# Kernel optimization log

Measured on AMD Instinct MI355X. Metric: run time of the kernel, lower is better.

The kernel has to match this reference:

```python
import jax, jax.numpy as jnp
import numpy as np

N_KW, N_RT = 100000, 20000
D, H, O = 128, 128, 128
E_A, E_B, E_C = 1600000, 1600000, 320000


def setup_inputs() -> dict:
    key = jax.random.key(0)
    ks = jax.random.split(key, 32)
    inp = {
        "x_kw": jax.random.normal(ks[0], (N_KW, D), jnp.float32),
        "x_rt": jax.random.normal(ks[1], (N_RT, D), jnp.float32),
        "src_a": jax.random.randint(ks[2], (E_A,), 0, N_RT),
        "dst_a": jax.random.randint(ks[3], (E_A,), 0, N_KW),
        "src_b": jax.random.randint(ks[4], (E_B,), 0, N_KW),
        "dst_b": jax.random.randint(ks[5], (E_B,), 0, N_KW),
        "src_c": jax.random.randint(ks[6], (E_C,), 0, N_RT),
        "dst_c": jax.random.randint(ks[7], (E_C,), 0, N_RT),
    }
    # SAGEConv params per relation per layer: W_l (neighbor), b_l, W_r (root, no bias)
    i = 8
    dims = {1: (D, H), 2: (H, O)}
    for layer in (1, 2):
        din, dout = dims[layer]
        for rel in ("a", "b", "c"):
            inp[f"Wl{layer}{rel}"] = jax.random.normal(ks[i], (din, dout), jnp.float32) * 0.05; i += 1
            inp[f"bl{layer}{rel}"] = jnp.zeros((dout,), jnp.float32)
            inp[f"Wr{layer}{rel}"] = jax.random.normal(ks[i], (din, dout), jnp.float32) * 0.05; i += 1
    return inp


def _sage(x_src, x_dst, src, dst, Wl, bl, Wr):
    # PyG SAGEConv (mean aggr): lin_l(mean_j x_src[j]) + lin_r(x_dst)
    n = x_dst.shape[0]
    s = jax.ops.segment_sum(x_src[src], dst, num_segments=n)      # [n, din]
    cnt = jax.ops.segment_sum(jnp.ones_like(dst, dtype=x_src.dtype), dst, num_segments=n)
    mean = s / jnp.maximum(cnt, 1.0)[:, None]
    return mean @ Wl + bl + x_dst @ Wr


def reference(x_kw, x_rt, src_a, dst_a, src_b, dst_b, src_c, dst_c,
              Wl1a, bl1a, Wr1a, Wl1b, bl1b, Wr1b, Wl1c, bl1c, Wr1c,
              Wl2a, bl2a, Wr2a, Wl2b, bl2b, Wr2b, Wl2c, bl2c, Wr2c):
    # layer 1 (HeteroConv aggr='sum' over relations sharing a dst type)
    kw1 = (_sage(x_rt, x_kw, src_a, dst_a, Wl1a, bl1a, Wr1a)
           + _sage(x_kw, x_kw, src_b, dst_b, Wl1b, bl1b, Wr1b))
    rt1 = _sage(x_rt, x_rt, src_c, dst_c, Wl1c, bl1c, Wr1c)
    kw1 = jax.nn.relu(kw1)
    rt1 = jax.nn.relu(rt1)
    # layer 2
    kw2 = (_sage(rt1, kw1, src_a, dst_a, Wl2a, bl2a, Wr2a)
           + _sage(kw1, kw1, src_b, dst_b, Wl2b, bl2b, Wr2b))
    rt2 = _sage(rt1, rt1, src_c, dst_c, Wl2c, bl2c, Wr2c)
    return kw2, rt2
```

## Files before the change

### kernel.cpp

```cpp
#include <hip/hip_runtime.h>

typedef __attribute__((ext_vector_type(8))) short bf16x8;
typedef __attribute__((ext_vector_type(4))) float f32x4;
typedef __attribute__((ext_vector_type(2))) float f32x2;

static __device__ __forceinline__ unsigned short f2bf(float f) {
    unsigned int u = __float_as_uint(f);
    u += 0x7fffu + ((u >> 16) & 1u);
    return (unsigned short)(u >> 16);
}
static __device__ __forceinline__ float bf2f(unsigned short h) {
    return __uint_as_float(((unsigned int)h) << 16);
}

#define BSH 6
#define BUCKET 64
#define NBMAX 1600
#define CHSH 13


struct Rel {
    const int* src; const int* dst; int E; int nb; int Ndst;
    int hblk0, hnblk;
    int sblk0, snblk;
    int oblk0;
    int shift;
    int* bcnt; int* boff; int* bcur;
    unsigned* pairs; unsigned* ssrc; int* goff; float* invd;
};
struct Rels { Rel r[3]; };

struct PrepArgs {
    const float* W[10];
    const float* Wa[10];
    const float* b1a; const float* b1b; const float* b2a; const float* b2b;
};


__global__ void prep_hist_k(PrepArgs pa, unsigned short* __restrict__ Wt,
                            float* __restrict__ bc1, float* __restrict__ bc2,
                            Rels R, int prepBlocks) {
    int bid = blockIdx.x;
    if (bid < prepBlocks) {
        if (bid < 640) {
            int slot = bid >> 6;
            int i = ((bid & 63) << 8) + threadIdx.x;
            float v = pa.W[slot][i];
            const float* w2 = pa.Wa[slot];
            if (w2) v += w2[i];
            int k = i >> 7, n = i & 127;
            Wt[slot * 16384 + n * 128 + k] = f2bf(v);
        } else {
            int t = threadIdx.x;
            if (t < 128) bc1[t] = pa.b1a[t] + pa.b1b[t];
            else bc2[t - 128] = pa.b2a[t - 128] + pa.b2b[t - 128];
        }
        return;
    }
    int hb = bid - prepBlocks;
    const Rel* r;
    if (hb < R.r[1].hblk0) r = &R.r[0];
    else if (hb < R.r[2].hblk0) r = &R.r[1];
    else r = &R.r[2];
    __shared__ int h[NBMAX];
    for (int i = threadIdx.x; i < r->nb; i += 256) h[i] = 0;
    __syncthreads();
    for (int e = (hb - r->hblk0) * 256 + threadIdx.x; e < r->E; e += r->hnblk * 256)
        atomicAdd(&h[r->dst[e] >> BSH], 1);
    __syncthreads();
    for (int i = threadIdx.x; i < r->nb; i += 256)
        if (h[i]) atomicAdd(&r->bcnt[i], h[i]);
}


__global__ void bscan3_k(Rels R) {
    const Rel* r = &R.r[blockIdx.x];
    __shared__ int s[1024];
    int t = threadIdx.x;
    int nb = r->nb;
    int e0 = 2 * t, e1 = 2 * t + 1;
    int v0 = (e0 < nb) ? r->bcnt[e0] : 0;
    int v1 = (e1 < nb) ? r->bcnt[e1] : 0;
    s[t] = v0 + v1;
    __syncthreads();
    for (int o = 1; o < 1024; o <<= 1) {
        int x = (t >= o) ? s[t - o] : 0;
        __syncthreads();
        s[t] += x;
        __syncthreads();
    }
    int P = s[t] - (v0 + v1);
    if (e0 <= nb) { r->boff[e0] = P; if (e0 < nb) r->bcur[e0] = 0; }
    if (e1 <= nb) { r->boff[e1] = P + v0; if (e1 < nb) r->bcur[e1] = 0; }
}

__global__ __launch_bounds__(256) void bscatter3_k(Rels R) {
    const Rel* r;
    int bid = blockIdx.x;
    if (bid < R.r[1].sblk0) r = &R.r[0];
    else if (bid < R.r[2].sblk0) r = &R.r[1];
    else r = &R.r[2];
    __shared__ int h[NBMAX];
    __shared__ int base[NBMAX];
    int t = threadIdx.x;
    int nb = r->nb, E = r->E;
    for (int i = t; i < nb; i += 256) h[i] = 0;
    __syncthreads();
    int e0 = (bid - r->sblk0) * 8192;
    for (int i = 0; i < 32; i++) {
        int e = e0 + i * 256 + t;
        if (e < E) atomicAdd(&h[r->dst[e] >> BSH], 1);
    }
    __syncthreads();
    for (int i = t; i < nb; i += 256) {
        int c = h[i];
        base[i] = c ? (r->boff[i] + atomicAdd(&r->bcur[i], c)) : 0;
    }
    __syncthreads();
    for (int i = t; i < nb; i += 256) h[i] = 0;
    __syncthreads();
    for (int i = 0; i < 32; i++) {
        int e = e0 + i * 256 + t;
        if (e < E) {
            int d = r->dst[e];
            int b = d >> BSH;
            int pos = base[b] + atomicAdd(&h[b], 1);
            r->pairs[pos] = ((unsigned)(d & (BUCKET - 1)) << 17) | (unsigned)r->src[e];
        }
    }
}

static __device__ void sortb_body(const Rels& R, int bid) {
    const Rel* r;
    if (bid < R.r[1].oblk0) r = &R.r[0];
    else if (bid < R.r[2].oblk0) r = &R.r[1];
    else r = &R.r[2];
    int b = bid - r->oblk0;
    __shared__ int cnt[1024];
    __shared__ int sc[256];
    int t = threadIdx.x;
    for (int i = t; i < 1024; i += 256) cnt[i] = 0;
    __syncthreads();
    int j0 = r->boff[b], j1 = r->boff[b + 1];
    for (int j = j0 + t; j < j1; j += 256) {
        unsigned p = r->pairs[j];
        int d = (p >> 17) & 63;
        int ch = (int)((p & 0x1ffffu) >> CHSH); if (ch > 15) ch = 15;
        int bin = ((d & 7) << 7) | ((d >> 3) << 4) | ch;
        atomicAdd(&cnt[bin], 1);
    }
    __syncthreads();
    if (t < 64) {
        int b0 = ((t & 7) << 7) | ((t >> 3) << 4);
        int c = 0;
#pragma unroll
        for (int i = 0; i < 16; i++) c += cnt[b0 + i];
        int dd = (b << BSH) + t;
        if (dd < r->Ndst) r->invd[dd] = 1.f / (float)(c > 0 ? c : 1);
    }
    int c0 = cnt[4 * t], c1 = cnt[4 * t + 1], c2 = cnt[4 * t + 2], c3 = cnt[4 * t + 3];
    int tot = c0 + c1 + c2 + c3;
    sc[t] = tot;
    __syncthreads();
    for (int o = 1; o < 256; o <<= 1) {
        int x = (t >= o) ? sc[t - o] : 0;
        __syncthreads();
        sc[t] += x;
        __syncthreads();
    }
    int base = j0 + sc[t] - tot;
    if ((t & 3) == 0) r->goff[b * 64 + (t >> 2)] = base;
    cnt[4 * t] = base;
    cnt[4 * t + 1] = base + c0;
    cnt[4 * t + 2] = base + c0 + c1;
    cnt[4 * t + 3] = base + c0 + c1 + c2;
    if (t == 0 && b == r->nb - 1) r->goff[r->nb * 64] = r->E;
    __syncthreads();
    int shift = r->shift;
    for (int j = j0 + t; j < j1; j += 256) {
        unsigned p = r->pairs[j];
        int d = (p >> 17) & 63;
        int ch = (int)((p & 0x1ffffu) >> CHSH); if (ch > 15) ch = 15;
        int bin = ((d & 7) << 7) | ((d >> 3) << 4) | ch;
        int pos = atomicAdd(&cnt[bin], 1);
        r->ssrc[pos] = (p & 0x1ffffu) << shift;
    }
}


struct GemmJobs {
    const void* Akw; int Nkw;
    const unsigned short* Wk1; const float* bk; unsigned short* Zkw;
    const unsigned short* Wk2; unsigned char* Ckw8;
    const void* Art; int Nrt;
    const unsigned short* Wr1; const float* br; unsigned short* Zrt;
    const unsigned short* Wr2; unsigned short* Crt2;
    const unsigned short* Wr3; unsigned short* Crt3;
    int kwBlocks;
};

template <int AF32>
static __device__ void gemm_body(const GemmJobs& G, int bid) {
    bool iskw = bid < G.kwBlocks;
    const void* A = iskw ? G.Akw : G.Art;
    int N = iskw ? G.Nkw : G.Nrt;
    int lane = threadIdx.x & 63;
    int r16 = lane & 15, g = lane >> 4;
    int row0 = (iskw ? bid : bid - G.kwBlocks) * 64 + (threadIdx.x >> 6) * 16;
    int arow = row0 + r16;
    int arow_c = arow < N ? arow : N - 1;

    bf16x8 af[4];
    if (AF32) {
        const float* Af = (const float*)A + (size_t)arow_c * 128 + g * 8;
#pragma unroll
        for (int kc = 0; kc < 4; kc++) {
            float4 u0 = *(const float4*)(Af + kc * 32);
            float4 u1 = *(const float4*)(Af + kc * 32 + 4);
            bf16x8 rr;
            rr[0] = (short)f2bf(u0.x); rr[1] = (short)f2bf(u0.y);
            rr[2] = (short)f2bf(u0.z); rr[3] = (short)f2bf(u0.w);
            rr[4] = (short)f2bf(u1.x); rr[5] = (short)f2bf(u1.y);
            rr[6] = (short)f2bf(u1.z); rr[7] = (short)f2bf(u1.w);
            af[kc] = rr;
        }
    } else {
        const bf16x8* Ar = (const bf16x8*)((const unsigned short*)A + (size_t)arow_c * 128);
#pragma unroll
        for (int kc = 0; kc < 4; kc++) af[kc] = Ar[kc * 4 + g];
    }

    if (iskw) {
        f32x4 acc1[8], acc2[8];
#pragma unroll
        for (int ct = 0; ct < 8; ct++) { f32x4 z = {0.f,0.f,0.f,0.f}; acc1[ct] = z; acc2[ct] = z; }
#pragma unroll
        for (int kc = 0; kc < 4; kc++) {
#pragma unroll
            for (int ct = 0; ct < 8; ct++) {
                int wo = ((ct * 16 + r16) << 7) + kc * 32 + g * 8;
                bf16x8 b1 = *(const bf16x8*)(G.Wk1 + wo);
                acc1[ct] = __builtin_amdgcn_mfma_f32_16x16x32_bf16(af[kc], b1, acc1[ct], 0, 0, 0);
                bf16x8 b2 = *(const bf16x8*)(G.Wk2 + wo);
                acc2[ct] = __builtin_amdgcn_mfma_f32_16x16x32_bf16(af[kc], b2, acc2[ct], 0, 0, 0);
            }
        }
#pragma unroll
        for (int ct = 0; ct < 8; ct++) {
            int col = ct * 16 + r16;
            float bb = G.bk[col];
#pragma unroll
            for (int j = 0; j < 4; j++) {
                int r = row0 + g * 4 + j;
                if (r < N) {
                    G.Zkw[(size_t)r * 128 + col] = f2bf(acc1[ct][j] + bb);
                    float v2 = acc2[ct][j];
                    int pk = __builtin_amdgcn_cvt_pk_fp8_f32(v2, v2, 0, false);
                    G.Ckw8[(size_t)r * 128 + col] = (unsigned char)(pk & 0xff);
                }
            }
        }
    } else {
        f32x4 acc1[8], acc2[8], acc3[8];
#pragma unroll
        for (int ct = 0; ct < 8; ct++) {
            f32x4 z = {0.f,0.f,0.f,0.f}; acc1[ct] = z; acc2[ct] = z; acc3[ct] = z;
        }
#pragma unroll
        for (int kc = 0; kc < 4; kc++) {
#pragma unroll
            for (int ct = 0; ct < 8; ct++) {
                int wo = ((ct * 16 + r16) << 7) + kc * 32 + g * 8;
                bf16x8 b1 = *(const bf16x8*)(G.Wr1 + wo);
                acc1[ct] = __builtin_amdgcn_mfma_f32_16x16x32_bf16(af[kc], b1, acc1[ct], 0, 0, 0);
                bf16x8 b2 = *(const bf16x8*)(G.Wr2 + wo);
                acc2[ct] = __builtin_amdgcn_mfma_f32_16x16x32_bf16(af[kc], b2, acc2[ct], 0, 0, 0);
                bf16x8 b3 = *(const bf16x8*)(G.Wr3 + wo);
                acc3[ct] = __builtin_amdgcn_mfma_f32_16x16x32_bf16(af[kc], b3, acc3[ct], 0, 0, 0);
            }
        }
#pragma unroll
        for (int ct = 0; ct < 8; ct++) {
            int col = ct * 16 + r16;
            float bb = G.br[col];
#pragma unroll
            for (int j = 0; j < 4; j++) {
                int r = row0 + g * 4 + j;
                if (r < N) {
                    G.Zrt[(size_t)r * 128 + col] = f2bf(acc1[ct][j] + bb);
                    G.Crt2[(size_t)r * 128 + col] = f2bf(acc2[ct][j]);
                    G.Crt3[(size_t)r * 128 + col] = f2bf(acc3[ct][j]);
                }
            }
        }
    }
}

__global__ __launch_bounds__(256) void gemm_sort_k(GemmJobs G, Rels R, int gemmBlocks) {
    if ((int)blockIdx.x < gemmBlocks) gemm_body<1>(G, blockIdx.x);
    else sortb_body(R, blockIdx.x - gemmBlocks);
}

__global__ __launch_bounds__(256) void gemm_l2_k(GemmJobs G) {
    gemm_body<0>(G, blockIdx.x);
}

template <int FMT>
static __device__ __forceinline__ void row_accum(const unsigned* __restrict__ spw, int len,
                                                 const char* __restrict__ Y, int lb, int h,
                                                 f32x2& a01, f32x2& a23) {
    int j = 0;
#pragma unroll 1
    for (; j + 16 <= len; j += 16) {
        unsigned o[8];
#pragma unroll
        for (int k = 0; k < 8; k++) {
            unsigned oe = spw[j + 2 * k];
            unsigned oo = spw[j + 2 * k + 1];
            o[k] = h ? oo : oe;
        }
        if (FMT == 0) {
            uint2 v[8];
#pragma unroll
            for (int k = 0; k < 8; k++) v[k] = *(const uint2*)(Y + o[k] + lb);
#pragma unroll
            for (int k = 0; k < 8; k++) {
                f32x2 x01 = { __uint_as_float(v[k].x << 16), __uint_as_float(v[k].x & 0xffff0000u) };
                f32x2 x23 = { __uint_as_float(v[k].y << 16), __uint_as_float(v[k].y & 0xffff0000u) };
                a01 += x01; a23 += x23;
            }
        } else {
            unsigned v[8];
#pragma unroll
            for (int k = 0; k < 8; k++) v[k] = *(const unsigned*)(Y + o[k] + lb);
#pragma unroll
            for (int k = 0; k < 8; k++) {
                auto lo = __builtin_amdgcn_cvt_pk_f32_fp8(v[k], false);
                auto hi = __builtin_amdgcn_cvt_pk_f32_fp8(v[k], true);
                a01[0] += lo[0]; a01[1] += lo[1];
                a23[0] += hi[0]; a23[1] += hi[1];
            }
        }
    }
    if (j < len) {
#pragma unroll
        for (int k = 0; k < 8; k++) {
            int e = j + 2 * k + h;
            int ec = e < len ? e : len - 1;
            bool live = e < len;
            unsigned o = spw[ec];
            if (FMT == 0) {
                uint2 v = *(const uint2*)(Y + o + lb);
                unsigned vx = live ? v.x : 0u, vy = live ? v.y : 0u;
                f32x2 x01 = { __uint_as_float(vx << 16), __uint_as_float(vx & 0xffff0000u) };
                f32x2 x23 = { __uint_as_float(vy << 16), __uint_as_float(vy & 0xffff0000u) };
                a01 += x01; a23 += x23;
            } else {
                unsigned vv = *(const unsigned*)(Y + o + lb);
                vv = live ? vv : 0u;
                auto lo = __builtin_amdgcn_cvt_pk_f32_fp8(vv, false);
                auto hi = __builtin_amdgcn_cvt_pk_f32_fp8(vv, true);
                a01[0] += lo[0]; a01[1] += lo[1];
                a23[0] += hi[0]; a23[1] += hi[1];
            }
        }
    }
}

template <int FMT>
static __device__ __forceinline__ void agg_rel(float* acc, int b, int w, int h, int q,
                                               int dst0,
                                               const unsigned* __restrict__ sp,
                                               const int* __restrict__ goff,
                                               const float* __restrict__ invd,
                                               const char* __restrict__ Ybase) {
    int lb = FMT ? (q << 2) : (q << 3);
#pragma unroll 1
    for (int r = 0; r < 8; r++) {
        int gi = b * 64 + w * 8 + r;
        int jg0 = __builtin_amdgcn_readfirstlane(goff[gi]);
        int jg1 = __builtin_amdgcn_readfirstlane(goff[gi + 1]);
        if (jg0 >= jg1) continue;
        int d = (r << 3) | w;
        f32x2 a01 = {0.f, 0.f}, a23 = {0.f, 0.f};
        row_accum<FMT>(sp + jg0, jg1 - jg0, Ybase, lb, h, a01, a23);
        a01[0] += __shfl_xor(a01[0], 32);
        a01[1] += __shfl_xor(a01[1], 32);
        a23[0] += __shfl_xor(a23[0], 32);
        a23[1] += __shfl_xor(a23[1], 32);
        float inv = invd[dst0 + d];
        float v0 = (h ? a23[0] : a01[0]) * inv;
        float v1 = (h ? a23[1] : a01[1]) * inv;
        int ba = d * 128 + q + h * 64;
        acc[ba] += v0;
        acc[ba + 32] += v1;
    }
}

struct AggJob {
    const unsigned short* Zin; int Ndst;
    const unsigned* sp0; const int* goff0; const float* invd0; const void* Y0; int fmt0;
    const unsigned* sp1; const int* goff1; const float* invd1; const void* Y1; int fmt1;
    int nrel;
    float* OutF; unsigned short* OutB;
};

template <int RELU, int OUTBF16>
__global__ __launch_bounds__(512) void bagg2_k(AggJob JK, AggJob JR, int kwBlocks) {
    __shared__ float acc[BUCKET * 128];
    bool iskw = blockIdx.x < (unsigned)kwBlocks;
    AggJob J = iskw ? JK : JR;
    int b = iskw ? blockIdx.x : blockIdx.x - kwBlocks;
    int t = threadIdx.x;
    int dst0 = b << BSH;
    int nrow = J.Ndst - dst0; if (nrow > BUCKET) nrow = BUCKET;

    for (int c = t; c < BUCKET * 32; c += 512) {
        int r = c >> 5, m = c & 31;
        float z0 = 0.f, z1 = 0.f, z2 = 0.f, z3 = 0.f;
        if (r < nrow) {
            ushort4 z = *(const ushort4*)(J.Zin + (size_t)(dst0 + r) * 128 + (m << 2));
            z0 = bf2f(z.x); z1 = bf2f(z.y); z2 = bf2f(z.z); z3 = bf2f(z.w);
        }
        acc[r * 128 + m] = z0;
        acc[r * 128 + 32 + m] = z1;
        acc[r * 128 + 64 + m] = z2;
        acc[r * 128 + 96 + m] = z3;
    }
    __syncthreads();

    int w = t >> 6, lane = t & 63;
    int h = lane >> 5, q = lane & 31;
    if (J.fmt0 == 0) agg_rel<0>(acc, b, w, h, q, dst0, J.sp0, J.goff0, J.invd0, (const char*)J.Y0);
    else agg_rel<1>(acc, b, w, h, q, dst0, J.sp0, J.goff0, J.invd0, (const char*)J.Y0);
    if (J.nrel == 2) {
        if (J.fmt1 == 0) agg_rel<0>(acc, b, w, h, q, dst0, J.sp1, J.goff1, J.invd1, (const char*)J.Y1);
        else agg_rel<1>(acc, b, w, h, q, dst0, J.sp1, J.goff1, J.invd1, (const char*)J.Y1);
    }
    __syncthreads();
    for (int c = t; c < BUCKET * 32; c += 512) {
        int r = c >> 5, m = c & 31;
        if (r < nrow) {
            float x0 = acc[r * 128 + m];
            float x1 = acc[r * 128 + 32 + m];
            float x2 = acc[r * 128 + 64 + m];
            float x3 = acc[r * 128 + 96 + m];
            if (RELU) {
                x0 = fmaxf(x0, 0.f); x1 = fmaxf(x1, 0.f);
                x2 = fmaxf(x2, 0.f); x3 = fmaxf(x3, 0.f);
            }
            size_t o = (size_t)(dst0 + r) * 128 + (m << 2);
            if (OUTBF16) {
                ushort4 ov;
                ov.x = f2bf(x0); ov.y = f2bf(x1); ov.z = f2bf(x2); ov.w = f2bf(x3);
                *(ushort4*)(J.OutB + o) = ov;
            } else {
                *(float4*)(J.OutF + o) = make_float4(x0, x1, x2, x3);
            }
        }
    }
}


static inline size_t align256(size_t x) { return (x + 255) & ~size_t(255); }

extern "C" void kernel_launch(void* const* d_in, const int* in_sizes, int n_in,
                              void* d_out, int out_size, void* d_ws, size_t ws_size,
                              hipStream_t stream) {
    const float* x_kw = (const float*)d_in[0];
    const float* x_rt = (const float*)d_in[1];
    const int* src_a = (const int*)d_in[2];
    const int* dst_a = (const int*)d_in[3];
    const int* src_b = (const int*)d_in[4];
    const int* dst_b = (const int*)d_in[5];
    const int* src_c = (const int*)d_in[6];
    const int* dst_c = (const int*)d_in[7];
    const float *Wl1a = (const float*)d_in[8],  *bl1a = (const float*)d_in[9],  *Wr1a = (const float*)d_in[10];
    const float *Wl1b = (const float*)d_in[11], *bl1b = (const float*)d_in[12], *Wr1b = (const float*)d_in[13];
    const float *Wl1c = (const float*)d_in[14], *bl1c = (const float*)d_in[15], *Wr1c = (const float*)d_in[16];
    const float *Wl2a = (const float*)d_in[17], *bl2a = (const float*)d_in[18], *Wr2a = (const float*)d_in[19];
    const float *Wl2b = (const float*)d_in[20], *bl2b = (const float*)d_in[21], *Wr2b = (const float*)d_in[22];
    const float *Wl2c = (const float*)d_in[23], *bl2c = (const float*)d_in[24], *Wr2c = (const float*)d_in[25];

    const int NKW = in_sizes[0] / 128;
    const int NRT = in_sizes[1] / 128;
    const int EA = in_sizes[2], EB = in_sizes[4], EC = in_sizes[6];
    const int nb_kw = (NKW + BUCKET - 1) / BUCKET;
    const int nb_rt = (NRT + BUCKET - 1) / BUCKET;

    char* ws = (char*)d_ws;
    size_t off = 0;
    auto alloc = [&](size_t bytes) -> char* {
        off = align256(off);
        char* p = ws + off;
        off += bytes;
        return p;
    };
    unsigned short* Wt = (unsigned short*)alloc(10 * 16384 * 2);
    float* bc1 = (float*)alloc(128 * 4);
    float* bc2 = (float*)alloc(128 * 4);
    int* bcnt3 = (int*)alloc(3 * NBMAX * 4);
    int* bcur3 = (int*)alloc(3 * NBMAX * 4);
    int* boff_a = (int*)alloc((NBMAX + 1) * 4);
    int* boff_b = (int*)alloc((NBMAX + 1) * 4);
    int* boff_c = (int*)alloc((NBMAX + 1) * 4);
    int* goff_a = (int*)alloc(((size_t)nb_kw * 64 + 1) * 4);
    int* goff_b = (int*)alloc(((size_t)nb_kw * 64 + 1) * 4);
    int* goff_c = (int*)alloc(((size_t)nb_rt * 64 + 1) * 4);
    float* invd_a = (float*)alloc((size_t)NKW * 4);
    float* invd_b = (float*)alloc((size_t)NKW * 4);
    float* invd_c = (float*)alloc((size_t)NRT * 4);
    unsigned* pairs_a = (unsigned*)alloc((size_t)EA * 4);
    unsigned* pairs_b = (unsigned*)alloc((size_t)EB * 4);
    unsigned* pairs_c = (unsigned*)alloc((size_t)EC * 4);
    unsigned* sp_a = (unsigned*)alloc((size_t)EA * 4);
    unsigned* sp_b = (unsigned*)alloc((size_t)EB * 4);
    unsigned* sp_c = (unsigned*)alloc((size_t)EC * 4);
    unsigned short* Ya = (unsigned short*)alloc((size_t)NRT * 128 * 2);
    unsigned char*  Yb = (unsigned char*)alloc((size_t)NKW * 128);
    unsigned short* Yc = (unsigned short*)alloc((size_t)NRT * 128 * 2);
    unsigned short* Zkw = (unsigned short*)alloc((size_t)NKW * 128 * 2);
    unsigned short* Zrt = (unsigned short*)alloc((size_t)NRT * 128 * 2);
    unsigned short* kw1_bf = (unsigned short*)alloc((size_t)NKW * 128 * 2);
    unsigned short* rt1_bf = (unsigned short*)alloc((size_t)NRT * 128 * 2);
    (void)ws_size;

    float* out_kw = (float*)d_out;
    float* out_rt = out_kw + (size_t)NKW * 128;

    Rels R;
    int hA = 128, hB = 128, hC = 64;
    int sA = (EA + 8191) / 8192, sB = (EB + 8191) / 8192, sC = (EC + 8191) / 8192;
    R.r[0] = {src_a, dst_a, EA, nb_kw, NKW, 0, hA, 0, sA, 0, 8,
              bcnt3, boff_a, bcur3, pairs_a, sp_a, goff_a, invd_a};
    R.r[1] = {src_b, dst_b, EB, nb_kw, NKW, hA, hB, sA, sB, nb_kw, 7,
              bcnt3 + NBMAX, boff_b, bcur3 + NBMAX, pairs_b, sp_b, goff_b, invd_b};
    R.r[2] = {src_c, dst_c, EC, nb_rt, NRT, hA + hB, hC, sA + sB, sC, 2 * nb_kw, 8,
              bcnt3 + 2 * NBMAX, boff_c, bcur3 + 2 * NBMAX, pairs_c, sp_c, goff_c, invd_c};

    hipMemsetAsync(bcnt3, 0, 3 * NBMAX * 4, stream);
    PrepArgs pa;
    pa.W[0] = Wr1a; pa.Wa[0] = Wr1b;
    pa.W[1] = Wl1a; pa.Wa[1] = nullptr;
    pa.W[2] = Wl1b; pa.Wa[2] = nullptr;
    pa.W[3] = Wl1c; pa.Wa[3] = nullptr;
    pa.W[4] = Wr1c; pa.Wa[4] = nullptr;
    pa.W[5] = Wr2a; pa.Wa[5] = Wr2b;
    pa.W[6] = Wl2a; pa.Wa[6] = nullptr;
    pa.W[7] = Wl2b; pa.Wa[7] = nullptr;
    pa.W[8] = Wl2c; pa.Wa[8] = nullptr;
    pa.W[9] = Wr2c; pa.Wa[9] = nullptr;
    pa.b1a = bl1a; pa.b1b = bl1b; pa.b2a = bl2a; pa.b2b = bl2b;
    prep_hist_k<<<641 + hA + hB + hC, 256, 0, stream>>>(pa, Wt, bc1, bc2, R, 641);
    unsigned short* W0 = Wt + 0 * 16384;
    unsigned short* W1 = Wt + 1 * 16384;
    unsigned short* W2 = Wt + 2 * 16384;
    unsigned short* W3 = Wt + 3 * 16384;
    unsigned short* W4 = Wt + 4 * 16384;
    unsigned short* W5 = Wt + 5 * 16384;
    unsigned short* W6 = Wt + 6 * 16384;
    unsigned short* W7 = Wt + 7 * 16384;
    unsigned short* W8 = Wt + 8 * 16384;
    unsigned short* W9 = Wt + 9 * 16384;

    bscan3_k<<<3, 1024, 0, stream>>>(R);
    bscatter3_k<<<sA + sB + sC, 256, 0, stream>>>(R);

    const int kwB = (NKW + 63) / 64, rtB = (NRT + 63) / 64;
    const int nsort = 2 * nb_kw + nb_rt;

    GemmJobs G1;
    G1.Akw = x_kw; G1.Nkw = NKW; G1.Wk1 = W0; G1.bk = bc1; G1.Zkw = Zkw; G1.Wk2 = W2; G1.Ckw8 = Yb;
    G1.Art = x_rt; G1.Nrt = NRT; G1.Wr1 = W4; G1.br = bl1c; G1.Zrt = Zrt;
    G1.Wr2 = W1; G1.Crt2 = Ya; G1.Wr3 = W3; G1.Crt3 = Yc;
    G1.kwBlocks = kwB;
    gemm_sort_k<<<kwB + rtB + nsort, 256, 0, stream>>>(G1, R, kwB + rtB);

    AggJob JK1 = {Zkw, NKW, sp_a, goff_a, invd_a, Ya, 0, sp_b, goff_b, invd_b, Yb, 1, 2,
                  nullptr, kw1_bf};
    AggJob JR1 = {Zrt, NRT, sp_c, goff_c, invd_c, Yc, 0, nullptr, nullptr, nullptr, nullptr, 0, 1,
                  nullptr, rt1_bf};
    bagg2_k<1, 1><<<nb_kw + nb_rt, 512, 0, stream>>>(JK1, JR1, nb_kw);

    GemmJobs G2;
    G2.Akw = kw1_bf; G2.Nkw = NKW; G2.Wk1 = W5; G2.bk = bc2; G2.Zkw = Zkw; G2.Wk2 = W7; G2.Ckw8 = Yb;
    G2.Art = rt1_bf; G2.Nrt = NRT; G2.Wr1 = W9; G2.br = bl2c; G2.Zrt = Zrt;
    G2.Wr2 = W6; G2.Crt2 = Ya; G2.Wr3 = W8; G2.Crt3 = Yc;
    G2.kwBlocks = kwB;
    gemm_l2_k<<<kwB + rtB, 256, 0, stream>>>(G2);

    AggJob JK2 = {Zkw, NKW, sp_a, goff_a, invd_a, Ya, 0, sp_b, goff_b, invd_b, Yb, 1, 2,
                  out_kw, nullptr};
    AggJob JR2 = {Zrt, NRT, sp_c, goff_c, invd_c, Yc, 0, nullptr, nullptr, nullptr, nullptr, 0, 1,
                  out_rt, nullptr};
    bagg2_k<0, 0><<<nb_kw + nb_rt, 512, 0, stream>>>(JK2, JR2, nb_kw);
}
```

Measured before the change: 586.3 us.

## Interleave gather streams of two relations or two rows in aggregation

```diff
diff --git a/kernel.cpp b/kernel.cpp
--- a/kernel.cpp
+++ b/kernel.cpp
@@ -305,96 +305,90 @@
     gemm_body<0>(G, blockIdx.x);
 }
 
-template <int FMT>
-static __device__ __forceinline__ void row_accum(const unsigned* __restrict__ spw, int len,
-                                                 const char* __restrict__ Y, int lb, int h,
+
+template <int F>
+static __device__ __forceinline__ void acc_batch(const uint2* v, const unsigned* wv,
                                                  f32x2& a01, f32x2& a23) {
-    int j = 0;
-#pragma unroll 1
-    for (; j + 16 <= len; j += 16) {
-        unsigned o[8];
-#pragma unroll
-        for (int k = 0; k < 8; k++) {
-            unsigned oe = spw[j + 2 * k];
-            unsigned oo = spw[j + 2 * k + 1];
-            o[k] = h ? oo : oe;
-        }
-        if (FMT == 0) {
-            uint2 v[8];
-#pragma unroll
-            for (int k = 0; k < 8; k++) v[k] = *(const uint2*)(Y + o[k] + lb);
+#pragma unroll
+    for (int k = 0; k < 8; k++) {
+        if (F == 0) {
+            f32x2 x01 = { __uint_as_float(v[k].x << 16), __uint_as_float(v[k].x & 0xffff0000u) };
+            f32x2 x23 = { __uint_as_float(v[k].y << 16), __uint_as_float(v[k].y & 0xffff0000u) };
+            a01 += x01; a23 += x23;
+        } else {
+            auto lo = __builtin_amdgcn_cvt_pk_f32_fp8(wv[k], false);
+            auto hi = __builtin_amdgcn_cvt_pk_f32_fp8(wv[k], true);
+            a01[0] += lo[0]; a01[1] += lo[1];
+            a23[0] += hi[0]; a23[1] += hi[1];
+        }
+    }
+}
+
+template <int F>
+static __device__ __forceinline__ void tail_accum(const unsigned* __restrict__ spw,
+                                                  int j, int len,
+                                                  const char* __restrict__ Y, int lb, int h,
+                                                  f32x2& a01, f32x2& a23) {
+    if (j >= len) return;
+#pragma unroll
+    for (int k = 0; k < 8; k++) {
+        int e = j + 2 * k + h;
+        int ec = e < len ? e : len - 1;
+        bool live = e < len;
+        unsigned o = spw[ec];
+        if (F == 0) {
+            uint2 v = *(const uint2*)(Y + o + lb);
+            unsigned vx = live ? v.x : 0u, vy = live ? v.y : 0u;
+            f32x2 x01 = { __uint_as_float(vx << 16), __uint_as_float(vx & 0xffff0000u) };
+            f32x2 x23 = { __uint_as_float(vy << 16), __uint_as_float(vy & 0xffff0000u) };
+            a01 += x01; a23 += x23;
+        } else {
+            unsigned vv = *(const unsigned*)(Y + o + lb);
+            vv = live ? vv : 0u;
+            auto lo = __builtin_amdgcn_cvt_pk_f32_fp8(vv, false);
+            auto hi = __builtin_amdgcn_cvt_pk_f32_fp8(vv, true);
+            a01[0] += lo[0]; a01[1] += lo[1];
+            a23[0] += hi[0]; a23[1] += hi[1];
+        }
+    }
+}
+
+template <int F0, int F1>
+static __device__ __forceinline__ void dual_accum(
+    const unsigned* __restrict__ sp0, int len0, const char* __restrict__ Y0, int lb0,
+    const unsigned* __restrict__ sp1, int len1, const char* __restrict__ Y1, int lb1,
+    int h, f32x2& p01, f32x2& p23, f32x2& q01, f32x2& q23) {
+    int nf0 = len0 & ~15, nf1 = len1 & ~15;
+    int j0 = 0, j1 = 0;
+    while (j0 < nf0 || j1 < nf1) {
+        bool g0 = j0 < nf0, g1 = j1 < nf1;
+        uint2 v0[8]; unsigned w0[8];
+        uint2 v1[8]; unsigned w1[8];
+        if (g0) {
 #pragma unroll
             for (int k = 0; k < 8; k++) {
-                f32x2 x01 = { __uint_as_float(v[k].x << 16), __uint_as_float(v[k].x & 0xffff0000u) };
-                f32x2 x23 = { __uint_as_float(v[k].y << 16), __uint_as_float(v[k].y & 0xffff0000u) };
-                a01 += x01; a23 += x23;
-            }
-        } else {
-            unsigned v[8];
-#pragma unroll
-            for (int k = 0; k < 8; k++) v[k] = *(const unsigned*)(Y + o[k] + lb);
+                unsigned oe = sp0[j0 + 2 * k];
+                unsigned oo = sp0[j0 + 2 * k + 1];
+                unsigned o = h ? oo : oe;
+                if (F0 == 0) v0[k] = *(const uint2*)(Y0 + o + lb0);
+                else w0[k] = *(const unsigned*)(Y0 + o + lb0);
+            }
+        }
+        if (g1) {
 #pragma unroll
             for (int k = 0; k < 8; k++) {
-                auto lo = __builtin_amdgcn_cvt_pk_f32_fp8(v[k], false);
-                auto hi = __builtin_amdgcn_cvt_pk_f32_fp8(v[k], true);
-                a01[0] += lo[0]; a01[1] += lo[1];
-                a23[0] += hi[0]; a23[1] += hi[1];
-            }
-        }
-    }
-    if (j < len) {
-#pragma unroll
-        for (int k = 0; k < 8; k++) {
-            int e = j + 2 * k + h;
-            int ec = e < len ? e : len - 1;
-            bool live = e < len;
-            unsigned o = spw[ec];
-            if (FMT == 0) {
-                uint2 v = *(const uint2*)(Y + o + lb);
-                unsigned vx = live ? v.x : 0u, vy = live ? v.y : 0u;
-                f32x2 x01 = { __uint_as_float(vx << 16), __uint_as_float(vx & 0xffff0000u) };
-                f32x2 x23 = { __uint_as_float(vy << 16), __uint_as_float(vy & 0xffff0000u) };
-                a01 += x01; a23 += x23;
-            } else {
-                unsigned vv = *(const unsigned*)(Y + o + lb);
-                vv = live ? vv : 0u;
-                auto lo = __builtin_amdgcn_cvt_pk_f32_fp8(vv, false);
-                auto hi = __builtin_amdgcn_cvt_pk_f32_fp8(vv, true);
-                a01[0] += lo[0]; a01[1] += lo[1];
-                a23[0] += hi[0]; a23[1] += hi[1];
-            }
-        }
-    }
-}
-
-template <int FMT>
-static __device__ __forceinline__ void agg_rel(float* acc, int b, int w, int h, int q,
-                                               int dst0,
-                                               const unsigned* __restrict__ sp,
-                                               const int* __restrict__ goff,
-                                               const float* __restrict__ invd,
-                                               const char* __restrict__ Ybase) {
-    int lb = FMT ? (q << 2) : (q << 3);
-#pragma unroll 1
-    for (int r = 0; r < 8; r++) {
-        int gi = b * 64 + w * 8 + r;
-        int jg0 = __builtin_amdgcn_readfirstlane(goff[gi]);
-        int jg1 = __builtin_amdgcn_readfirstlane(goff[gi + 1]);
-        if (jg0 >= jg1) continue;
-        int d = (r << 3) | w;
-        f32x2 a01 = {0.f, 0.f}, a23 = {0.f, 0.f};
-        row_accum<FMT>(sp + jg0, jg1 - jg0, Ybase, lb, h, a01, a23);
-        a01[0] += __shfl_xor(a01[0], 32);
-        a01[1] += __shfl_xor(a01[1], 32);
-        a23[0] += __shfl_xor(a23[0], 32);
-        a23[1] += __shfl_xor(a23[1], 32);
-        float inv = invd[dst0 + d];
-        float v0 = (h ? a23[0] : a01[0]) * inv;
-        float v1 = (h ? a23[1] : a01[1]) * inv;
-        int ba = d * 128 + q + h * 64;
-        acc[ba] += v0;
-        acc[ba + 32] += v1;
-    }
+                unsigned oe = sp1[j1 + 2 * k];
+                unsigned oo = sp1[j1 + 2 * k + 1];
+                unsigned o = h ? oo : oe;
+                if (F1 == 0) v1[k] = *(const uint2*)(Y1 + o + lb1);
+                else w1[k] = *(const unsigned*)(Y1 + o + lb1);
+            }
+        }
+        if (g0) { acc_batch<F0>(v0, w0, p01, p23); j0 += 16; }
+        if (g1) { acc_batch<F1>(v1, w1, q01, q23); j1 += 16; }
+    }
+    tail_accum<F0>(sp0, nf0, len0, Y0, lb0, h, p01, p23);
+    tail_accum<F1>(sp1, nf1, len1, Y1, lb1, h, q01, q23);
 }
 
 struct AggJob {
@@ -431,11 +425,79 @@
 
     int w = t >> 6, lane = t & 63;
     int h = lane >> 5, q = lane & 31;
-    if (J.fmt0 == 0) agg_rel<0>(acc, b, w, h, q, dst0, J.sp0, J.goff0, J.invd0, (const char*)J.Y0);
-    else agg_rel<1>(acc, b, w, h, q, dst0, J.sp0, J.goff0, J.invd0, (const char*)J.Y0);
+    int lb0 = J.fmt0 ? (q << 2) : (q << 3);
+    int lb1 = J.fmt1 ? (q << 2) : (q << 3);
+
     if (J.nrel == 2) {
-        if (J.fmt1 == 0) agg_rel<0>(acc, b, w, h, q, dst0, J.sp1, J.goff1, J.invd1, (const char*)J.Y1);
-        else agg_rel<1>(acc, b, w, h, q, dst0, J.sp1, J.goff1, J.invd1, (const char*)J.Y1);
+#pragma unroll 1
+        for (int r = 0; r < 8; r++) {
+            int gi = b * 64 + w * 8 + r;
+            int a0 = __builtin_amdgcn_readfirstlane(J.goff0[gi]);
+            int a1 = __builtin_amdgcn_readfirstlane(J.goff0[gi + 1]);
+            int c0 = __builtin_amdgcn_readfirstlane(J.goff1[gi]);
+            int c1 = __builtin_amdgcn_readfirstlane(J.goff1[gi + 1]);
+            int lenA = a1 - a0, lenB = c1 - c0;
+            if (lenA <= 0 && lenB <= 0) continue;
+            int d = (r << 3) | w;
+            f32x2 p01 = {0.f,0.f}, p23 = {0.f,0.f}, q01 = {0.f,0.f}, q23 = {0.f,0.f};
+            dual_accum<0, 1>(J.sp0 + a0, lenA, (const char*)J.Y0, lb0,
+                             J.sp1 + c0, lenB, (const char*)J.Y1, lb1,
+                             h, p01, p23, q01, q23);
+            float invA = J.invd0[dst0 + d];
+            float invB = J.invd1[dst0 + d];
+            float s0 = p01[0] * invA + q01[0] * invB;
+            float s1 = p01[1] * invA + q01[1] * invB;
+            float s2 = p23[0] * invA + q23[0] * invB;
+            float s3 = p23[1] * invA + q23[1] * invB;
+            s0 += __shfl_xor(s0, 32);
+            s1 += __shfl_xor(s1, 32);
+            s2 += __shfl_xor(s2, 32);
+            s3 += __shfl_xor(s3, 32);
+            int ba = d * 128 + q + h * 64;
+            acc[ba] += h ? s2 : s0;
+            acc[ba + 32] += h ? s3 : s1;
+        }
+    } else {
+#pragma unroll 1
+        for (int rp = 0; rp < 4; rp++) {
+            int gi0 = b * 64 + w * 8 + rp;
+            int gi1 = gi0 + 4;
+            int a0 = __builtin_amdgcn_readfirstlane(J.goff0[gi0]);
+            int a1 = __builtin_amdgcn_readfirstlane(J.goff0[gi0 + 1]);
+            int c0 = __builtin_amdgcn_readfirstlane(J.goff0[gi1]);
+            int c1 = __builtin_amdgcn_readfirstlane(J.goff0[gi1 + 1]);
+            int len0 = a1 - a0, len1 = c1 - c0;
+            if (len0 <= 0 && len1 <= 0) continue;
+            int d0 = (rp << 3) | w, d1 = ((rp + 4) << 3) | w;
+            f32x2 p01 = {0.f,0.f}, p23 = {0.f,0.f}, q01 = {0.f,0.f}, q23 = {0.f,0.f};
+            dual_accum<0, 0>(J.sp0 + a0, len0, (const char*)J.Y0, lb0,
+                             J.sp0 + c0, len1, (const char*)J.Y0, lb0,
+                             h, p01, p23, q01, q23);
+            if (len0 > 0) {
+                float inv = J.invd0[dst0 + d0];
+                float s0 = p01[0] * inv, s1 = p01[1] * inv;
+                float s2 = p23[0] * inv, s3 = p23[1] * inv;
+                s0 += __shfl_xor(s0, 32);
+                s1 += __shfl_xor(s1, 32);
+                s2 += __shfl_xor(s2, 32);
+                s3 += __shfl_xor(s3, 32);
+                int ba = d0 * 128 + q + h * 64;
+                acc[ba] += h ? s2 : s0;
+                acc[ba + 32] += h ? s3 : s1;
+            }
+            if (len1 > 0) {
+                float inv = J.invd0[dst0 + d1];
+                float s0 = q01[0] * inv, s1 = q01[1] * inv;
+                float s2 = q23[0] * inv, s3 = q23[1] * inv;
+                s0 += __shfl_xor(s0, 32);
+                s1 += __shfl_xor(s1, 32);
+                s2 += __shfl_xor(s2, 32);
+                s3 += __shfl_xor(s3, 32);
+                int ba = d1 * 128 + q + h * 64;
+                acc[ba] += h ? s2 : s0;
+                acc[ba + 32] += h ? s3 : s1;
+            }
+        }
     }
     __syncthreads();
     for (int c = t; c < BUCKET * 32; c += 512) {
```

New measurement: 650.0 us. 1.11x slower.
